# Performance work log

Measured on AMD Instinct MI355X. Metric: run time of the kernel, lower is better.

## Reference

```python
import math
import jax, jax.numpy as jnp
import numpy as np

CAPACITY_FACTOR = 1.0
MIN_CAPACITY = 4


def setup_inputs() -> dict:
    key = jax.random.key(0)
    k1, k2 = jax.random.split(key)
    x = jax.random.normal(k1, (8192, 1024), dtype=jnp.float32)
    wg = jax.random.normal(k2, (1024, 64), dtype=jnp.float32) * 0.02
    return {"x": x, "wg": wg}


def reference(x, wg):
    # Gate projection: [S, D] @ [D, E] -> [S, E]
    logits = x @ wg
    S, E = logits.shape
    # _capacity: ceil(S / E * capacity_factor * 2) for top-2, floored at min_capacity (static)
    capacity = max(math.ceil((S / E) * (CAPACITY_FACTOR * 2.0)), MIN_CAPACITY)

    gates = jax.nn.softmax(logits, axis=-1)           # [S, E]
    org_gates = gates

    # top-1 expert
    indices1_s = jnp.argmax(gates, axis=1)
    mask1 = jax.nn.one_hot(indices1_s, E, dtype=jnp.int32)
    # top-2 expert (deterministic: no gumbel sampling)
    logits_except1 = jnp.where(mask1.astype(bool), -jnp.inf, logits)
    indices2_s = jnp.argmax(logits_except1, axis=1)
    mask2 = jax.nn.one_hot(indices2_s, E, dtype=jnp.int32)

    # per-expert running positions
    locations1 = jnp.cumsum(mask1, axis=0) - 1        # [S, E]
    locations2 = jnp.cumsum(mask2, axis=0) - 1 + jnp.sum(mask1, axis=0, keepdims=True)

    # load-balancing aux loss
    me = jnp.mean(gates, axis=0)
    ce = jnp.mean(mask1.astype(gates.dtype), axis=0)
    l_aux = jnp.sum(me * ce) * E * E

    exp_counts = jnp.sum(mask1 + mask2, axis=0)

    # drop tokens over capacity
    mask1 = mask1 * (locations1 < capacity).astype(jnp.int32)
    mask2 = mask2 * (locations2 < capacity).astype(jnp.int32)

    locations1_s = jnp.sum(locations1 * mask1, axis=1)  # [S]
    locations2_s = jnp.sum(locations2 * mask2, axis=1)

    mask1_f = mask1.astype(gates.dtype)
    mask2_f = mask2.astype(gates.dtype)
    gates1_s = jnp.sum(gates * mask1_f, axis=1)
    gates2_s = jnp.sum(gates * mask2_f, axis=1)
    denom_s = jnp.clip(gates1_s + gates2_s, jnp.finfo(gates.dtype).eps)
    gates1_s = gates1_s / denom_s
    gates2_s = gates2_s / denom_s

    gates1 = gates1_s[:, None] * mask1_f              # [S, E]
    gates2 = gates2_s[:, None] * mask2_f

    locations1_sc = jax.nn.one_hot(locations1_s, capacity, dtype=gates.dtype)  # [S, C]
    locations2_sc = jax.nn.one_hot(locations2_s, capacity, dtype=gates.dtype)

    combine_weights = (jnp.einsum('se,sc->sec', gates1, locations1_sc)
                       + jnp.einsum('se,sc->sec', gates2, locations2_sc))  # [S, E, C]
    dispatch_mask = combine_weights.astype(bool)
    return l_aux, combine_weights, dispatch_mask, exp_counts, org_gates
```

## Files before the change

### kernel.cpp

```cpp
#include <hip/hip_runtime.h>
#include <math.h>

#define S_TOKENS 8192
#define D_DIM    1024
#define E_EXP    64
#define CAPACITY 256
#define TPB      64
#define NBLK     (S_TOKENS / TPB)
#define NZBLK    4096

typedef float fx4 __attribute__((ext_vector_type(4)));

#define SZ_COMBINE   (134217728LL)
#define OFF_COMBINE  (1LL)
#define OFF_DISPATCH (OFF_COMBINE + SZ_COMBINE)
#define OFF_EXPCNT   (OFF_DISPATCH + SZ_COMBINE)
#define OFF_ORGGATES (OFF_EXPCNT + E_EXP)

#define WS_IDX1 0
#define WS_IDX2 (WS_IDX1 + S_TOKENS)
#define WS_G1   (WS_IDX2 + S_TOKENS)
#define WS_G2   (WS_G1 + S_TOKENS)
#define WS_CNT1 (WS_G2 + S_TOKENS)
#define WS_CNT2 (WS_CNT1 + NBLK * E_EXP)
#define WS_MEP  (WS_CNT2 + NBLK * E_EXP)

__global__ __launch_bounds__(256) void kA_gemm_fill(
    const float* __restrict__ x, const float* __restrict__ wg,
    float* __restrict__ out, int* __restrict__ wsi, float* __restrict__ wsf) {
  const int bid = blockIdx.x;
  const int tid = threadIdx.x;

  if (bid >= NBLK) {
    fx4 z = (fx4)0.f;
    fx4* p = (fx4*)out;
    const size_t n4 = (size_t)(2 * SZ_COMBINE) / 4;
    const size_t nth = (size_t)NZBLK * 256;
    for (size_t i = (size_t)(bid - NBLK) * 256 + tid; i < n4; i += nth)
      p[i] = z;
    if (bid == NBLK && tid == 0) out[2 * SZ_COMBINE] = 0.0f;
    return;
  }

  __shared__ float xs[64][68];
  __shared__ float ovl[64 * 68];
  __shared__ float mM[64], rS[64];
  __shared__ int   li1[64], li2[64];
  __shared__ float mered[16][64];

  float (*wsh)[64] = (float(*)[64])ovl;
  float (*Lg)[68]  = (float(*)[68])ovl;

  const int tx = tid & 15;
  const int ty = tid >> 4;
  const int s0 = bid * TPB;

  float acc[4][4];
#pragma unroll
  for (int i = 0; i < 4; i++)
#pragma unroll
    for (int q = 0; q < 4; q++) acc[i][q] = 0.f;

  for (int k0 = 0; k0 < D_DIM; k0 += 64) {
#pragma unroll
    for (int r = 0; r < 4; r++) {
      int i = tid + 256 * r;
      int t = i >> 4, c = i & 15;
      *(fx4*)&xs[t][4 * c] =
          *(const fx4*)&x[(size_t)(s0 + t) * D_DIM + k0 + 4 * c];
      *(fx4*)&wsh[t][4 * c] =
          *(const fx4*)&wg[(size_t)(k0 + t) * E_EXP + 4 * c];
    }
    __syncthreads();
    for (int kb = 0; kb < 64; kb += 4) {
      fx4 xa[4], wb[4];
#pragma unroll
      for (int i = 0; i < 4; i++) xa[i] = *(fx4*)&xs[ty + 16 * i][kb];
#pragma unroll
      for (int j = 0; j < 4; j++) wb[j] = *(fx4*)&wsh[kb + j][4 * tx];
#pragma unroll
      for (int j = 0; j < 4; j++)
#pragma unroll
        for (int i = 0; i < 4; i++) {
          float xv = xa[i][j];
#pragma unroll
          for (int q = 0; q < 4; q++)
            acc[i][q] = fmaf(xv, wb[j][q], acc[i][q]);
        }
    }
    __syncthreads();
  }

#pragma unroll
  for (int i = 0; i < 4; i++) {
    fx4 v;
#pragma unroll
    for (int q = 0; q < 4; q++) v[q] = acc[i][q];
    *(fx4*)&Lg[ty + 16 * i][4 * tx] = v;
  }
  __syncthreads();

  {
    const int g = tid >> 2;
    const int u = tid & 3;
    float bv = -INFINITY; int bi = 0;
#pragma unroll
    for (int i = 0; i < 16; i++) {
      int ee = u + 4 * i;
      float v = Lg[g][ee];
      if (v > bv) { bv = v; bi = ee; }
    }
#pragma unroll
    for (int d = 1; d < 4; d <<= 1) {
      float ovv = __shfl_xor(bv, d, 4);
      int   oi  = __shfl_xor(bi, d, 4);
      if (ovv > bv || (ovv == bv && oi < bi)) { bv = ovv; bi = oi; }
    }
    const float m1 = bv; const int i1 = bi;

    float se = 0.f;
#pragma unroll
    for (int i = 0; i < 16; i++) se += expf(Lg[g][u + 4 * i] - m1);
#pragma unroll
    for (int d = 1; d < 4; d <<= 1) se += __shfl_xor(se, d, 4);

    float bv2 = -INFINITY; int bi2 = 0;
#pragma unroll
    for (int i = 0; i < 16; i++) {
      int ee = u + 4 * i;
      float v = Lg[g][ee];
      if (ee != i1 && v > bv2) { bv2 = v; bi2 = ee; }
    }
#pragma unroll
    for (int d = 1; d < 4; d <<= 1) {
      float ovv = __shfl_xor(bv2, d, 4);
      int   oi  = __shfl_xor(bi2, d, 4);
      if (ovv > bv2 || (ovv == bv2 && oi < bi2)) { bv2 = ovv; bi2 = oi; }
    }

    if (u == 0) {
      float rs = 1.0f / se;
      mM[g] = m1; rS[g] = rs;
      li1[g] = i1; li2[g] = bi2;
      int s = s0 + g;
      wsi[WS_IDX1 + s] = i1;
      wsi[WS_IDX2 + s] = bi2;
      wsf[WS_G1 + s] = rs;
      wsf[WS_G2 + s] = expf(bv2 - m1) * rs;
    }
  }
  __syncthreads();

  {
    float ms[4] = {0.f, 0.f, 0.f, 0.f};
#pragma unroll
    for (int i = 0; i < 4; i++) {
      int t = ty + 16 * i;
      float m = mM[t], r = rS[t];
      size_t ob = OFF_ORGGATES + (size_t)(s0 + t) * E_EXP + 4 * tx;
#pragma unroll
      for (int q = 0; q < 4; q++) {
        float gate = expf(Lg[t][4 * tx + q] - m) * r;
        out[ob + q] = gate;
        ms[q] += gate;
      }
    }
#pragma unroll
    for (int q = 0; q < 4; q++) mered[ty][4 * tx + q] = ms[q];
  }
  __syncthreads();

  if (tid < 64) {
    float s = 0.f;
#pragma unroll
    for (int yy = 0; yy < 16; yy++) s += mered[yy][tid];
    wsf[WS_MEP + bid * 64 + tid] = s;
    int c1 = 0, c2 = 0;
    for (int t = 0; t < TPB; t++) {
      c1 += (li1[t] == tid);
      c2 += (li2[t] == tid);
    }
    wsi[WS_CNT1 + bid * 64 + tid] = c1;
    wsi[WS_CNT2 + bid * 64 + tid] = c2;
  }
}

__global__ __launch_bounds__(64) void kB_scan_scatter(
    float* __restrict__ out, const int* __restrict__ wsi,
    const float* __restrict__ wsf) {
  const int bid = blockIdx.x;
  const int e = threadIdx.x;

  if (bid == NBLK) {
    int t1 = 0, t2 = 0;
    float ms = 0.f;
#pragma unroll 8
    for (int c = 0; c < NBLK; c++) {
      t1 += wsi[WS_CNT1 + c * 64 + e];
      t2 += wsi[WS_CNT2 + c * 64 + e];
      ms += wsf[WS_MEP + c * 64 + e];
    }
    out[OFF_EXPCNT + e] = (float)(t1 + t2);
    float me = ms * (1.0f / 8192.0f);
    float ce = (float)t1 * (1.0f / 8192.0f);
    float prod = me * ce * 4096.0f;
#pragma unroll
    for (int d = 1; d < 64; d <<= 1) prod += __shfl_xor(prod, d, 64);
    if (e == 0) out[0] = prod;
    return;
  }

  __shared__ int soff1[64], soff2[64];
  __shared__ int li1[TPB], li2[TPB];

  {
    int o1 = 0, o2 = 0, t1 = 0;
#pragma unroll 8
    for (int c = 0; c < NBLK; c++) {
      int c1 = wsi[WS_CNT1 + c * 64 + e];
      t1 += c1;
      if (c < bid) {
        o1 += c1;
        o2 += wsi[WS_CNT2 + c * 64 + e];
      }
    }
    soff1[e] = o1;
    soff2[e] = t1 + o2;
  }

  const int t = e;
  const int s0 = bid * TPB;
  li1[t] = wsi[WS_IDX1 + s0 + t];
  li2[t] = wsi[WS_IDX2 + s0 + t];
  __syncthreads();

  const int e1 = li1[t], e2 = li2[t];
  int r1 = 0, r2 = 0;
  for (int j = 0; j < t; j++) {
    r1 += (li1[j] == e1);
    r2 += (li2[j] == e2);
  }
  const int loc1 = soff1[e1] + r1;
  const int loc2 = soff2[e2] + r2;
  const int s = s0 + t;

  const float g1r = wsf[WS_G1 + s];
  const float g2r = wsf[WS_G2 + s];
  const bool d1 = (loc1 >= CAPACITY);
  const bool d2 = (loc2 >= CAPACITY);
  const float g1f = d1 ? 0.f : g1r;
  const float g2f = d2 ? 0.f : g2r;
  const float denom = fmaxf(g1f + g2f, 1.1920929e-7f);
  const float w1 = g1f / denom;
  const float w2 = g2f / denom;

  if (!d1) {
    size_t o = OFF_COMBINE + (size_t)s * (E_EXP * CAPACITY) +
               (size_t)e1 * CAPACITY + loc1;
    out[o] = w1;
    out[o + SZ_COMBINE] = (w1 != 0.f) ? 1.f : 0.f;
  }
  if (!d2) {
    size_t o = OFF_COMBINE + (size_t)s * (E_EXP * CAPACITY) +
               (size_t)e2 * CAPACITY + loc2;
    out[o] = w2;
    out[o + SZ_COMBINE] = (w2 != 0.f) ? 1.f : 0.f;
  }
}

extern "C" void kernel_launch(void* const* d_in, const int* in_sizes, int n_in,
                              void* d_out, int out_size, void* d_ws,
                              size_t ws_size, hipStream_t stream) {
  const float* x  = (const float*)d_in[0];
  const float* wg = (const float*)d_in[1];
  float* out = (float*)d_out;
  int*   wsi = (int*)d_ws;
  float* wsf = (float*)d_ws;

  hipLaunchKernelGGL(kA_gemm_fill, dim3(NBLK + NZBLK), dim3(256), 0, stream,
                     x, wg, out, wsi, wsf);
  hipLaunchKernelGGL(kB_scan_scatter, dim3(NBLK + 1), dim3(64), 0, stream,
                     out, wsi, wsf);
}
```

Baseline: 1.163 ms.

## Fuse output zero-fill into per-chunk scatter kernel and halve tokens per block

Moves zeroing of the combine and dispatch tensors out of the GEMM kernel's extra fill blocks and into the second kernel. Each token chunk's block now zeroes its own output slab and then scatters its nonzero entries, so the scatter writes land right after the zeroing, possibly while still in cache. Tokens per block drop from 64 to 32, which doubles the number of GEMM and scatter blocks. The trade-off is that the whole fill now runs on only 257 blocks of 256 threads, roughly one per CU, which may not saturate store bandwidth. The fill also no longer overlaps with the GEMM.

```diff
diff --git a/kernel.cpp b/kernel.cpp
--- a/kernel.cpp
+++ b/kernel.cpp
@@ -5,9 +5,8 @@
 #define D_DIM    1024
 #define E_EXP    64
 #define CAPACITY 256
-#define TPB      64
-#define NBLK     (S_TOKENS / TPB)
-#define NZBLK    4096
+#define TPB      32
+#define NCHUNK   (S_TOKENS / TPB)
 
 typedef float fx4 __attribute__((ext_vector_type(4)));
 
@@ -22,30 +21,19 @@
 #define WS_G1   (WS_IDX2 + S_TOKENS)
 #define WS_G2   (WS_G1 + S_TOKENS)
 #define WS_CNT1 (WS_G2 + S_TOKENS)
-#define WS_CNT2 (WS_CNT1 + NBLK * E_EXP)
-#define WS_MEP  (WS_CNT2 + NBLK * E_EXP)
-
-__global__ __launch_bounds__(256) void kA_gemm_fill(
+#define WS_CNT2 (WS_CNT1 + NCHUNK * E_EXP)
+#define WS_MEP  (WS_CNT2 + NCHUNK * E_EXP)
+
+__global__ __launch_bounds__(256) void k1_gemm_gate(
     const float* __restrict__ x, const float* __restrict__ wg,
     float* __restrict__ out, int* __restrict__ wsi, float* __restrict__ wsf) {
   const int bid = blockIdx.x;
   const int tid = threadIdx.x;
 
-  if (bid >= NBLK) {
-    fx4 z = (fx4)0.f;
-    fx4* p = (fx4*)out;
-    const size_t n4 = (size_t)(2 * SZ_COMBINE) / 4;
-    const size_t nth = (size_t)NZBLK * 256;
-    for (size_t i = (size_t)(bid - NBLK) * 256 + tid; i < n4; i += nth)
-      p[i] = z;
-    if (bid == NBLK && tid == 0) out[2 * SZ_COMBINE] = 0.0f;
-    return;
-  }
-
-  __shared__ float xs[64][68];
+  __shared__ float xs[32][68];
   __shared__ float ovl[64 * 68];
-  __shared__ float mM[64], rS[64];
-  __shared__ int   li1[64], li2[64];
+  __shared__ float mM[32], rS[32];
+  __shared__ int   li1[32], li2[32];
   __shared__ float mered[16][64];
 
   float (*wsh)[64] = (float(*)[64])ovl;
@@ -55,33 +43,38 @@
   const int ty = tid >> 4;
   const int s0 = bid * TPB;
 
-  float acc[4][4];
-#pragma unroll
-  for (int i = 0; i < 4; i++)
+  float acc[2][4];
+#pragma unroll
+  for (int i = 0; i < 2; i++)
 #pragma unroll
     for (int q = 0; q < 4; q++) acc[i][q] = 0.f;
 
   for (int k0 = 0; k0 < D_DIM; k0 += 64) {
 #pragma unroll
-    for (int r = 0; r < 4; r++) {
+    for (int r = 0; r < 2; r++) {
       int i = tid + 256 * r;
       int t = i >> 4, c = i & 15;
       *(fx4*)&xs[t][4 * c] =
           *(const fx4*)&x[(size_t)(s0 + t) * D_DIM + k0 + 4 * c];
+    }
+#pragma unroll
+    for (int r = 0; r < 4; r++) {
+      int i = tid + 256 * r;
+      int t = i >> 4, c = i & 15;
       *(fx4*)&wsh[t][4 * c] =
           *(const fx4*)&wg[(size_t)(k0 + t) * E_EXP + 4 * c];
     }
     __syncthreads();
     for (int kb = 0; kb < 64; kb += 4) {
-      fx4 xa[4], wb[4];
-#pragma unroll
-      for (int i = 0; i < 4; i++) xa[i] = *(fx4*)&xs[ty + 16 * i][kb];
+      fx4 xa[2], wb[4];
+#pragma unroll
+      for (int i = 0; i < 2; i++) xa[i] = *(fx4*)&xs[ty + 16 * i][kb];
 #pragma unroll
       for (int j = 0; j < 4; j++) wb[j] = *(fx4*)&wsh[kb + j][4 * tx];
 #pragma unroll
       for (int j = 0; j < 4; j++)
 #pragma unroll
-        for (int i = 0; i < 4; i++) {
+        for (int i = 0; i < 2; i++) {
           float xv = xa[i][j];
 #pragma unroll
           for (int q = 0; q < 4; q++)
@@ -92,7 +85,7 @@
   }
 
 #pragma unroll
-  for (int i = 0; i < 4; i++) {
+  for (int i = 0; i < 2; i++) {
     fx4 v;
 #pragma unroll
     for (int q = 0; q < 4; q++) v[q] = acc[i][q];
@@ -103,50 +96,52 @@
   {
     const int g = tid >> 2;
     const int u = tid & 3;
-    float bv = -INFINITY; int bi = 0;
-#pragma unroll
-    for (int i = 0; i < 16; i++) {
-      int ee = u + 4 * i;
-      float v = Lg[g][ee];
-      if (v > bv) { bv = v; bi = ee; }
-    }
-#pragma unroll
-    for (int d = 1; d < 4; d <<= 1) {
-      float ovv = __shfl_xor(bv, d, 4);
-      int   oi  = __shfl_xor(bi, d, 4);
-      if (ovv > bv || (ovv == bv && oi < bi)) { bv = ovv; bi = oi; }
-    }
-    const float m1 = bv; const int i1 = bi;
-
-    float se = 0.f;
-#pragma unroll
-    for (int i = 0; i < 16; i++) se += expf(Lg[g][u + 4 * i] - m1);
-#pragma unroll
-    for (int d = 1; d < 4; d <<= 1) se += __shfl_xor(se, d, 4);
-
-    float bv2 = -INFINITY; int bi2 = 0;
-#pragma unroll
-    for (int i = 0; i < 16; i++) {
-      int ee = u + 4 * i;
-      float v = Lg[g][ee];
-      if (ee != i1 && v > bv2) { bv2 = v; bi2 = ee; }
-    }
-#pragma unroll
-    for (int d = 1; d < 4; d <<= 1) {
-      float ovv = __shfl_xor(bv2, d, 4);
-      int   oi  = __shfl_xor(bi2, d, 4);
-      if (ovv > bv2 || (ovv == bv2 && oi < bi2)) { bv2 = ovv; bi2 = oi; }
-    }
-
-    if (u == 0) {
-      float rs = 1.0f / se;
-      mM[g] = m1; rS[g] = rs;
-      li1[g] = i1; li2[g] = bi2;
-      int s = s0 + g;
-      wsi[WS_IDX1 + s] = i1;
-      wsi[WS_IDX2 + s] = bi2;
-      wsf[WS_G1 + s] = rs;
-      wsf[WS_G2 + s] = expf(bv2 - m1) * rs;
+    if (g < 32) {
+      float bv = -INFINITY; int bi = 0;
+#pragma unroll
+      for (int i = 0; i < 16; i++) {
+        int ee = u + 4 * i;
+        float v = Lg[g][ee];
+        if (v > bv) { bv = v; bi = ee; }
+      }
+#pragma unroll
+      for (int d = 1; d < 4; d <<= 1) {
+        float ovv = __shfl_xor(bv, d, 4);
+        int   oi  = __shfl_xor(bi, d, 4);
+        if (ovv > bv || (ovv == bv && oi < bi)) { bv = ovv; bi = oi; }
+      }
+      const float m1 = bv; const int i1 = bi;
+
+      float se = 0.f;
+#pragma unroll
+      for (int i = 0; i < 16; i++) se += expf(Lg[g][u + 4 * i] - m1);
+#pragma unroll
+      for (int d = 1; d < 4; d <<= 1) se += __shfl_xor(se, d, 4);
+
+      float bv2 = -INFINITY; int bi2 = 0;
+#pragma unroll
+      for (int i = 0; i < 16; i++) {
+        int ee = u + 4 * i;
+        float v = Lg[g][ee];
+        if (ee != i1 && v > bv2) { bv2 = v; bi2 = ee; }
+      }
+#pragma unroll
+      for (int d = 1; d < 4; d <<= 1) {
+        float ovv = __shfl_xor(bv2, d, 4);
+        int   oi  = __shfl_xor(bi2, d, 4);
+        if (ovv > bv2 || (ovv == bv2 && oi < bi2)) { bv2 = ovv; bi2 = oi; }
+      }
+
+      if (u == 0) {
+        float rs = 1.0f / se;
+        mM[g] = m1; rS[g] = rs;
+        li1[g] = i1; li2[g] = bi2;
+        int s = s0 + g;
+        wsi[WS_IDX1 + s] = i1;
+        wsi[WS_IDX2 + s] = bi2;
+        wsf[WS_G1 + s] = rs;
+        wsf[WS_G2 + s] = expf(bv2 - m1) * rs;
+      }
     }
   }
   __syncthreads();
@@ -154,7 +149,7 @@
   {
     float ms[4] = {0.f, 0.f, 0.f, 0.f};
 #pragma unroll
-    for (int i = 0; i < 4; i++) {
+    for (int i = 0; i < 2; i++) {
       int t = ty + 16 * i;
       float m = mM[t], r = rS[t];
       size_t ob = OFF_ORGGATES + (size_t)(s0 + t) * E_EXP + 4 * tx;
@@ -185,41 +180,49 @@
   }
 }
 
-__global__ __launch_bounds__(64) void kB_scan_scatter(
+__global__ __launch_bounds__(256) void kB_write(
     float* __restrict__ out, const int* __restrict__ wsi,
     const float* __restrict__ wsf) {
-  const int bid = blockIdx.x;
-  const int e = threadIdx.x;
-
-  if (bid == NBLK) {
-    int t1 = 0, t2 = 0;
-    float ms = 0.f;
+  const int b = blockIdx.x;
+  const int tid = threadIdx.x;
+
+  if (b == NCHUNK) {
+    if (tid < 64) {
+      const int e = tid;
+      int t1 = 0, t2 = 0;
+      float ms = 0.f;
 #pragma unroll 8
-    for (int c = 0; c < NBLK; c++) {
-      t1 += wsi[WS_CNT1 + c * 64 + e];
-      t2 += wsi[WS_CNT2 + c * 64 + e];
-      ms += wsf[WS_MEP + c * 64 + e];
-    }
-    out[OFF_EXPCNT + e] = (float)(t1 + t2);
-    float me = ms * (1.0f / 8192.0f);
-    float ce = (float)t1 * (1.0f / 8192.0f);
-    float prod = me * ce * 4096.0f;
-#pragma unroll
-    for (int d = 1; d < 64; d <<= 1) prod += __shfl_xor(prod, d, 64);
-    if (e == 0) out[0] = prod;
+      for (int c = 0; c < NCHUNK; c++) {
+        t1 += wsi[WS_CNT1 + c * 64 + e];
+        t2 += wsi[WS_CNT2 + c * 64 + e];
+        ms += wsf[WS_MEP + c * 64 + e];
+      }
+      out[OFF_EXPCNT + e] = (float)(t1 + t2);
+      float me = ms * (1.0f / 8192.0f);
+      float ce = (float)t1 * (1.0f / 8192.0f);
+      float prod = me * ce * 4096.0f;
+#pragma unroll
+      for (int d = 1; d < 64; d <<= 1) prod += __shfl_xor(prod, d, 64);
+      if (e == 0) out[0] = prod;
+    }
     return;
   }
 
   __shared__ int soff1[64], soff2[64];
-  __shared__ int li1[TPB], li2[TPB];
-
-  {
+  __shared__ int sli1[TPB], sli2[TPB];
+
+  if (tid < TPB) {
+    sli1[tid] = wsi[WS_IDX1 + b * TPB + tid];
+    sli2[tid] = wsi[WS_IDX2 + b * TPB + tid];
+  }
+  if (tid < 64) {
+    const int e = tid;
     int o1 = 0, o2 = 0, t1 = 0;
 #pragma unroll 8
-    for (int c = 0; c < NBLK; c++) {
+    for (int c = 0; c < NCHUNK; c++) {
       int c1 = wsi[WS_CNT1 + c * 64 + e];
       t1 += c1;
-      if (c < bid) {
+      if (c < b) {
         o1 += c1;
         o2 += wsi[WS_CNT2 + c * 64 + e];
       }
@@ -227,44 +230,73 @@
     soff1[e] = o1;
     soff2[e] = t1 + o2;
   }
-
-  const int t = e;
-  const int s0 = bid * TPB;
-  li1[t] = wsi[WS_IDX1 + s0 + t];
-  li2[t] = wsi[WS_IDX2 + s0 + t];
-  __syncthreads();
-
-  const int e1 = li1[t], e2 = li2[t];
-  int r1 = 0, r2 = 0;
-  for (int j = 0; j < t; j++) {
-    r1 += (li1[j] == e1);
-    r2 += (li2[j] == e2);
-  }
-  const int loc1 = soff1[e1] + r1;
-  const int loc2 = soff2[e2] + r2;
-  const int s = s0 + t;
-
-  const float g1r = wsf[WS_G1 + s];
-  const float g2r = wsf[WS_G2 + s];
-  const bool d1 = (loc1 >= CAPACITY);
-  const bool d2 = (loc2 >= CAPACITY);
-  const float g1f = d1 ? 0.f : g1r;
-  const float g2f = d2 ? 0.f : g2r;
-  const float denom = fmaxf(g1f + g2f, 1.1920929e-7f);
-  const float w1 = g1f / denom;
-  const float w2 = g2f / denom;
-
-  if (!d1) {
-    size_t o = OFF_COMBINE + (size_t)s * (E_EXP * CAPACITY) +
-               (size_t)e1 * CAPACITY + loc1;
-    out[o] = w1;
-    out[o + SZ_COMBINE] = (w1 != 0.f) ? 1.f : 0.f;
-  }
-  if (!d2) {
-    size_t o = OFF_COMBINE + (size_t)s * (E_EXP * CAPACITY) +
-               (size_t)e2 * CAPACITY + loc2;
-    out[o] = w2;
-    out[o + SZ_COMBINE] = (w2 != 0.f) ? 1.f : 0.f;
+  __syncthreads();
+
+  bool kept1 = false, kept2 = false;
+  size_t o1f = 0, o2f = 0;
+  float w1 = 0.f, w2 = 0.f;
+  if (tid < TPB) {
+    const int t = tid;
+    const int e1 = sli1[t], e2 = sli2[t];
+    int r1 = 0, r2 = 0;
+    for (int j = 0; j < t; j++) {
+      r1 += (sli1[j] == e1);
+      r2 += (sli2[j] == e2);
+    }
+    const int loc1 = soff1[e1] + r1;
+    const int loc2 = soff2[e2] + r2;
+    const int s = b * TPB + t;
+
+    const float g1r = wsf[WS_G1 + s];
+    const float g2r = wsf[WS_G2 + s];
+    const bool d1 = (loc1 >= CAPACITY);
+    const bool d2 = (loc2 >= CAPACITY);
+    const float g1f = d1 ? 0.f : g1r;
+    const float g2f = d2 ? 0.f : g2r;
+    const float denom = fmaxf(g1f + g2f, 1.1920929e-7f);
+    w1 = g1f / denom;
+    w2 = g2f / denom;
+    kept1 = !d1;
+    kept2 = !d2;
+    o1f = OFF_COMBINE + (size_t)s * (E_EXP * CAPACITY) +
+          (size_t)e1 * CAPACITY + loc1;
+    o2f = OFF_COMBINE + (size_t)s * (E_EXP * CAPACITY) +
+          (size_t)e2 * CAPACITY + loc2;
+  }
+
+  {
+    const size_t RB = (size_t)TPB * E_EXP * CAPACITY;
+    const size_t base = (size_t)b * RB;
+    fx4* cb4 = (fx4*)(out + base + 4);
+    fx4* db4 = cb4 + (SZ_COMBINE / 4);
+    const fx4 z = (fx4)0.f;
+#pragma unroll 4
+    for (int r = 0; r < 512; r++) {
+      int m = tid + 256 * r;
+      if (m < 131071) {
+        cb4[m] = z;
+        db4[m] = z;
+      }
+    }
+    if (tid < 3) {
+      out[base + 1 + tid] = 0.f;
+      out[SZ_COMBINE + base + 1 + tid] = 0.f;
+    } else if (tid == 3) {
+      out[base + RB] = 0.f;
+      out[SZ_COMBINE + base + RB] = 0.f;
+    }
+  }
+  __syncthreads();
+
+  if (tid < TPB) {
+    if (kept1) {
+      out[o1f] = w1;
+      out[o1f + SZ_COMBINE] = (w1 != 0.f) ? 1.f : 0.f;
+    }
+    if (kept2) {
+      out[o2f] = w2;
+      out[o2f + SZ_COMBINE] = (w2 != 0.f) ? 1.f : 0.f;
+    }
   }
 }
 
@@ -277,8 +309,8 @@
   int*   wsi = (int*)d_ws;
   float* wsf = (float*)d_ws;
 
-  hipLaunchKernelGGL(kA_gemm_fill, dim3(NBLK + NZBLK), dim3(256), 0, stream,
+  hipLaunchKernelGGL(k1_gemm_gate, dim3(NCHUNK), dim3(256), 0, stream,
                      x, wg, out, wsi, wsf);
-  hipLaunchKernelGGL(kB_scan_scatter, dim3(NBLK + 1), dim3(64), 0, stream,
+  hipLaunchKernelGGL(kB_write, dim3(NCHUNK + 1), dim3(256), 0, stream,
                      out, wsi, wsf);
 }
```

Result: no change. 1.170 ms (+0.6%).
